# Optimization experiments

Hardware: AMD Instinct MI355X
Metric: run time of the kernel (lower is better)

## Reference

```python
import jax, jax.numpy as jnp
import numpy as np

B, T, E, H, M2 = 8, 2048, 256, 2, 134
HD = E // H


def setup_inputs() -> dict:
    key = jax.random.key(0)
    ks = jax.random.split(key, 10)
    s = 0.02
    return {
        "X": jax.random.normal(ks[0], (B, T, E), dtype=jnp.float32),
        "Y": jax.random.uniform(ks[1], (B, M2), dtype=jnp.float32),
        "wpe": s * jax.random.normal(ks[2], (T, E), dtype=jnp.float32),
        "ln1_g": jnp.ones((E,), jnp.float32), "ln1_b": jnp.zeros((E,), jnp.float32),
        "attn_w": s * jax.random.normal(ks[3], (3 * E, E), dtype=jnp.float32),
        "attn_b": jnp.zeros((3 * E,), jnp.float32),
        "attnproj_w": s * jax.random.normal(ks[4], (E, E), dtype=jnp.float32),
        "attnproj_b": jnp.zeros((E,), jnp.float32),
        "ln2_g": jnp.ones((E,), jnp.float32), "ln2_b": jnp.zeros((E,), jnp.float32),
        "fc_w": s * jax.random.normal(ks[5], (2 * E, E), dtype=jnp.float32),
        "fc_b": jnp.zeros((2 * E,), jnp.float32),
        "mlpproj_w": s * jax.random.normal(ks[6], (E, 2 * E), dtype=jnp.float32),
        "mlpproj_b": jnp.zeros((E,), jnp.float32),
        "lnf_g": jnp.ones((E,), jnp.float32), "lnf_b": jnp.zeros((E,), jnp.float32),
        "head_w": s * jax.random.normal(ks[7], (M2, E), dtype=jnp.float32),
        "head_b": jnp.zeros((M2,), jnp.float32),
    }


def _ln(x, g, b, eps=1e-5):
    mu = x.mean(-1, keepdims=True)
    var = ((x - mu) ** 2).mean(-1, keepdims=True)
    return (x - mu) * jax.lax.rsqrt(var + eps) * g + b


def reference(X, Y, wpe, ln1_g, ln1_b, attn_w, attn_b, attnproj_w, attnproj_b,
              ln2_g, ln2_b, fc_w, fc_b, mlpproj_w, mlpproj_b, lnf_g, lnf_b,
              head_w, head_b):
    # positional ids = arange(T) -> wpe itself; cls ids = [0]*T/2 + [1]*T/2
    cls_ids = np.concatenate([np.zeros(T // 2, np.int32), np.ones(T // 2, np.int32)])
    x = X + wpe + wpe[cls_ids]                      # [B,T,E] (dropout = identity, eval)

    # single Block (n_layer=1), preceded by ReLU as in cross_mod loop
    x = jax.nn.relu(x)
    h = _ln(x, ln1_g, ln1_b)
    qkv = h @ attn_w.T + attn_b                     # [B,T,3E]
    q, k, v = jnp.split(qkv, 3, axis=-1)
    q, k, v = jax.nn.relu(q), jax.nn.relu(k), jax.nn.relu(v)
    split_heads = lambda t: t.reshape(B, T, H, HD).transpose(0, 2, 1, 3)
    q, k, v = split_heads(q), split_heads(k), split_heads(v)
    att = jnp.einsum('bhqd,bhkd->bhqk', q, k) * (1.0 / np.sqrt(HD))
    tril = jnp.tril(jnp.ones((T, T), dtype=bool))
    # masked_fill(-inf) then ReLU  ==  zero outside causal mask, ReLU inside
    att = jnp.where(tril, jax.nn.relu(att), 0.0)    # [B,H,T,T]
    y = jnp.einsum('bhqk,bhkd->bhqd', att, v)
    y = y.transpose(0, 2, 1, 3).reshape(B, T, E)
    x = x + (y @ attnproj_w.T + attnproj_b)

    h = _ln(x, ln2_g, ln2_b)
    x = x + (jax.nn.relu(h @ fc_w.T + fc_b) @ mlpproj_w.T + mlpproj_b)

    x = jax.nn.relu(x)
    x = _ln(x, lnf_g, lnf_b)
    x = jax.nn.relu(x)
    emb = x.mean(axis=1)                            # [B,E]
    logits = jax.nn.relu(emb @ head_w.T + head_b)   # [B,M2]

    loss1 = jnp.sqrt(jnp.mean((logits - Y) ** 2))
    e1, e2 = emb[:, : E // 2], emb[:, E // 2:]
    loss3 = jnp.sqrt(jnp.mean((e1 - e2) ** 2))
    loss = 50.0 * loss1 + loss3
    return (e1, e2, loss, loss1, loss3, logits)
```

## Files before the change

### kernel.cpp

```cpp
#include <hip/hip_runtime.h>
#include <hip/hip_bf16.h>

#define Bc 8
#define Tc 2048
#define Ec 256
#define Hc 2
#define HDc 128
#define Mrows (Bc*Tc)
#define M2c 134

using bfx8  = __attribute__((ext_vector_type(8))) __bf16;
using f32x4 = __attribute__((ext_vector_type(4))) float;

__device__ __forceinline__ void gll16(const __bf16* g, __bf16* lds) {
    __builtin_amdgcn_global_load_lds(
        (const __attribute__((address_space(1))) unsigned int*)g,
        (__attribute__((address_space(3))) unsigned int*)lds, 16, 0, 0);
}

__global__ __launch_bounds__(256) void embed_prep_k(const float* X, const float* wpe,
                                                    const float* g, const float* bb,
                                                    const float* attn_w, const float* apw,
                                                    const float* fcw, const float* mpw,
                                                    __bf16* wb, float* embsum,
                                                    __bf16* xres, __bf16* hb) {
    int m = blockIdx.x;
    int e = threadIdx.x;
    if (m < 2048) {
        int i = m * 256 + e;
        if (i < 196608)       wb[i] = (__bf16)attn_w[i];
        else if (i < 262144)  wb[i] = (__bf16)apw[i - 196608];
        else if (i < 393216)  wb[i] = (__bf16)fcw[i - 262144];
        else                  wb[i] = (__bf16)mpw[i - 393216];
        if (m < 8) embsum[m * 256 + e] = 0.f;
    }
    int t = m & (Tc - 1);
    float v = X[(size_t)m * Ec + e] + wpe[(size_t)t * Ec + e] + wpe[(size_t)(t >= 1024) * Ec + e];
    v = fmaxf(v, 0.f);
    xres[(size_t)m * Ec + e] = (__bf16)v;
    float s1 = v, s2 = v * v;
    #pragma unroll
    for (int o = 32; o; o >>= 1) { s1 += __shfl_xor(s1, o, 64); s2 += __shfl_xor(s2, o, 64); }
    __shared__ float a1[4], a2[4];
    int w = threadIdx.x >> 6;
    if ((threadIdx.x & 63) == 0) { a1[w] = s1; a2[w] = s2; }
    __syncthreads();
    float m1 = (a1[0] + a1[1] + a1[2] + a1[3]) * (1.f / 256.f);
    float m2 = (a2[0] + a2[1] + a2[2] + a2[3]) * (1.f / 256.f);
    float r = rsqrtf(m2 - m1 * m1 + 1e-5f);
    hb[(size_t)m * Ec + e] = (__bf16)((v - m1) * r * g[e] + bb[e]);
}

__global__ __launch_bounds__(256) void gemm_qkv(const __bf16* __restrict__ A,
                                                const __bf16* __restrict__ Bw,
                                                const float* __restrict__ bias,
                                                __bf16* __restrict__ Qb,
                                                __bf16* __restrict__ Kb,
                                                __bf16* __restrict__ Vb) {
    const int K = 256;
    __shared__ __bf16 As[128 * 64];
    __shared__ __bf16 Bs[128 * 64];
    const int tid = threadIdx.x, w = tid >> 6, l = tid & 63;
    const int m0 = blockIdx.y * 128, n0 = blockIdx.x * 128;
    const int wr = w >> 1, wc = w & 1;
    const int quad = l >> 4, col15 = l & 15;

    f32x4 acc[4][4];
    f32x4 zz = {0.f, 0.f, 0.f, 0.f};
    #pragma unroll
    for (int i = 0; i < 4; i++)
        #pragma unroll
        for (int j = 0; j < 4; j++) acc[i][j] = zz;

    const int lrow = l >> 3;
    const int pbs  = l & 7;

    for (int kb = 0; kb < K; kb += 64) {
        #pragma unroll
        for (int it = 0; it < 4; it++) {
            int chunk = w * 4 + it;
            int row = chunk * 8 + lrow;
            int lb = pbs ^ (row & 7);
            gll16(A  + (size_t)(m0 + row) * K + kb + lb * 8, As + chunk * 512);
            gll16(Bw + (size_t)(n0 + row) * K + kb + lb * 8, Bs + chunk * 512);
        }
        __syncthreads();
        #pragma unroll
        for (int ks = 0; ks < 2; ks++) {
            bfx8 af[4], bfr[4];
            #pragma unroll
            for (int rt = 0; rt < 4; rt++) {
                int row = wr * 64 + rt * 16 + col15;
                int pb = (ks * 4 + quad) ^ (row & 7);
                af[rt] = *(const bfx8*)(As + row * 64 + pb * 8);
            }
            #pragma unroll
            for (int ct = 0; ct < 4; ct++) {
                int row = wc * 64 + ct * 16 + col15;
                int pb = (ks * 4 + quad) ^ (row & 7);
                bfr[ct] = *(const bfx8*)(Bs + row * 64 + pb * 8);
            }
            #pragma unroll
            for (int rt = 0; rt < 4; rt++)
                #pragma unroll
                for (int ct = 0; ct < 4; ct++)
                    acc[rt][ct] = __builtin_amdgcn_mfma_f32_16x16x32_bf16(af[rt], bfr[ct], acc[rt][ct], 0, 0, 0);
        }
        __syncthreads();
    }

    #pragma unroll
    for (int rt = 0; rt < 4; rt++)
        #pragma unroll
        for (int ct = 0; ct < 4; ct++) {
            int mgb = m0 + wr * 64 + rt * 16 + quad * 4;
            int ng  = n0 + wc * 64 + ct * 16 + col15;
            float bsv = bias[ng];
            #pragma unroll
            for (int r = 0; r < 4; r++) {
                float val = fmaxf(acc[rt][ct][r] + bsv, 0.f);
                int mg = mgb + r;
                int sel = ng >> 8;
                int hh = (ng >> 7) & 1;
                int d = ng & 127;
                int bb = mg >> 11, tt = mg & (Tc - 1);
                size_t idx = ((size_t)((bb * 2 + hh) * Tc + tt)) * HDc + d;
                __bf16 bv = (__bf16)val;
                if (sel == 0) Qb[idx] = bv;
                else if (sel == 1) Kb[idx] = bv;
                else Vb[idx] = bv;
            }
        }
}

__global__ __launch_bounds__(256) void transpose_v(const unsigned short* Vb, unsigned short* Vt) {
    __shared__ unsigned short tile[64][66];
    int kt = blockIdx.x, dt = blockIdx.y, bh = blockIdx.z;
    int tid = threadIdx.x;
    int k0 = kt * 64, d0 = dt * 64;
    int rr = tid >> 4, cc = (tid & 15) * 4;
    #pragma unroll
    for (int p = 0; p < 4; p++) {
        int k = p * 16 + rr;
        const unsigned short* src = Vb + ((size_t)(bh * Tc + k0 + k)) * HDc + d0 + cc;
        ushort4 vv = *(const ushort4*)src;
        tile[k][cc] = vv.x; tile[k][cc + 1] = vv.y; tile[k][cc + 2] = vv.z; tile[k][cc + 3] = vv.w;
    }
    __syncthreads();
    #pragma unroll
    for (int p = 0; p < 4; p++) {
        int d = p * 16 + rr;
        unsigned short* dst = Vt + ((size_t)(bh * HDc + d0 + d)) * Tc + k0 + cc;
        ushort4 ov;
        ov.x = tile[cc][d]; ov.y = tile[cc + 1][d]; ov.z = tile[cc + 2][d]; ov.w = tile[cc + 3][d];
        *(ushort4*)dst = ov;
    }
}

__global__ __launch_bounds__(256, 4) void attn6_k(const __bf16* __restrict__ Qb,
                                                  const __bf16* __restrict__ Kb,
                                                  const __bf16* __restrict__ Vt,
                                                  __bf16* __restrict__ Y1,
                                                  __bf16* __restrict__ Y2,
                                                  __bf16* __restrict__ Y3,
                                                  __bf16* __restrict__ Y4) {
    __shared__ __bf16 Ks[64 * 128];
    __shared__ __bf16 Vs[128 * 64];
    __shared__ __bf16 Ss[64 * 64];
    int bid = blockIdx.x;
    int lane8 = bid & 7;
    int s = bid >> 3;
    int bh = ((s & 1) << 3) | lane8;
    int f = s >> 1;
    int qt, ch;
    if (f < 8)       { qt = f;                    ch = 0; }
    else if (f < 24) { qt = 8 + ((f - 8) >> 1);   ch = (f - 8) & 1; }
    else if (f < 48) { int r = f - 24; int d3 = r / 3; qt = 16 + d3; ch = r - 3 * d3; }
    else             { int r = f - 48; qt = 24 + (r >> 2); ch = r & 3; }
    int Q0 = qt * 64;
    int kts = ch * 8;
    int kte = min(kts + 8, qt + 1);

    int tid = threadIdx.x, w = tid >> 6, l = tid & 63;
    int quad = l >> 4, col15 = l & 15;
    const int lrowK = l >> 4, pbsK = l & 15;
    const int lrowV = l >> 3, pbsV = l & 7;

    #pragma unroll
    for (int it = 0; it < 4; it++) {
        int chunk = w * 4 + it;
        int row = chunk * 4 + lrowK;
        int lb = pbsK ^ (row & 7);
        gll16(Qb + ((size_t)(bh * Tc + Q0 + row)) * HDc + lb * 8, Ks + chunk * 512);
    }
    __syncthreads();
    bfx8 qf[4];
    #pragma unroll
    for (int ks = 0; ks < 4; ks++) {
        int row = w * 16 + col15;
        int pb = (ks * 4 + quad) ^ (row & 7);
        qf[ks] = *(const bfx8*)(Ks + row * 128 + pb * 8);
    }

    f32x4 zz = {0.f, 0.f, 0.f, 0.f};
    f32x4 yacc[8];
    #pragma unroll
    for (int i = 0; i < 8; i++) yacc[i] = zz;

    for (int kt = kts; kt < kte; kt++) {
        __syncthreads();
        #pragma unroll
        for (int it = 0; it < 4; it++) {
            int chunk = w * 4 + it;
            int rowK = chunk * 4 + lrowK;
            int lbK = pbsK ^ (rowK & 7);
            gll16(Kb + ((size_t)(bh * Tc + kt * 64 + rowK)) * HDc + lbK * 8, Ks + chunk * 512);
            int rowV = chunk * 8 + lrowV;
            int lbV = pbsV ^ (rowV & 7);
            gll16(Vt + ((size_t)(bh * HDc + rowV)) * Tc + kt * 64 + lbV * 8, Vs + chunk * 512);
        }
        __syncthreads();

        f32x4 sacc[4];
        #pragma unroll
        for (int i = 0; i < 4; i++) sacc[i] = zz;
        #pragma unroll
        for (int ks = 0; ks < 4; ks++) {
            #pragma unroll
            for (int ct = 0; ct < 4; ct++) {
                int row = ct * 16 + col15;
                int pb = (ks * 4 + quad) ^ (row & 7);
                bfx8 kf = *(const bfx8*)(Ks + row * 128 + pb * 8);
                sacc[ct] = __builtin_amdgcn_mfma_f32_16x16x32_bf16(qf[ks], kf, sacc[ct], 0, 0, 0);
            }
        }

        #pragma unroll
        for (int ct = 0; ct < 4; ct++) {
            int kl = ct * 16 + col15;
            int kg = kt * 64 + kl;
            int blk = kl >> 3, off = kl & 7;
            #pragma unroll
            for (int r = 0; r < 4; r++) {
                int qlw = w * 16 + quad * 4 + r;
                float val = (kg <= Q0 + qlw) ? fmaxf(sacc[ct][r], 0.f) : 0.f;
                int pb = blk ^ (qlw & 7);
                Ss[qlw * 64 + pb * 8 + off] = (__bf16)val;
            }
        }

        #pragma unroll
        for (int ks = 0; ks < 2; ks++) {
            int rowS = w * 16 + col15;
            int pbS = (ks * 4 + quad) ^ (rowS & 7);
            bfx8 sf = *(const bfx8*)(Ss + rowS * 64 + pbS * 8);
            #pragma unroll
            for (int dt = 0; dt < 8; dt++) {
                int row = dt * 16 + col15;
                int pb = (ks * 4 + quad) ^ (row & 7);
                bfx8 vf = *(const bfx8*)(Vs + row * 64 + pb * 8);
                yacc[dt] = __builtin_amdgcn_mfma_f32_16x16x32_bf16(sf, vf, yacc[dt], 0, 0, 0);
            }
        }
    }

    __bf16* Yp = (ch == 0) ? Y1 : (ch == 1) ? Y2 : (ch == 2) ? Y3 : Y4;
    int b = bh >> 1, h = bh & 1;
    const float sc = 0.08838834764831845f;
    #pragma unroll
    for (int dt = 0; dt < 8; dt++) {
        int d = dt * 16 + col15;
        #pragma unroll
        for (int r = 0; r < 4; r++) {
            int q = Q0 + w * 16 + quad * 4 + r;
            Yp[((size_t)(b * Tc + q)) * Ec + h * HDc + d] = (__bf16)(yacc[dt][r] * sc);
        }
    }
}

__global__ __launch_bounds__(256, 1) void mega_k(const __bf16* __restrict__ Y1,
                                                 const __bf16* __restrict__ Y2,
                                                 const __bf16* __restrict__ Y3,
                                                 const __bf16* __restrict__ Y4,
                                                 const __bf16* __restrict__ wap,
                                                 const float* __restrict__ apb,
                                                 const __bf16* __restrict__ xres,
                                                 const float* __restrict__ ln2_g,
                                                 const float* __restrict__ ln2_b,
                                                 const __bf16* __restrict__ wfc,
                                                 const float* __restrict__ fcb,
                                                 const __bf16* __restrict__ wmp,
                                                 const float* __restrict__ mpb,
                                                 const float* __restrict__ lnf_g,
                                                 const float* __restrict__ lnf_b,
                                                 float* __restrict__ embsum) {
    __shared__ __bf16 h2s[4 * 4096];
    __shared__ __bf16 fc64[8 * 4096];
    __shared__ __bf16 Bs[256 * 64];
    __shared__ float cs[256];
    const int tid = threadIdx.x, w = tid >> 6, l = tid & 63;
    const int m0 = blockIdx.x * 64;
    const int quad = l >> 4, col15 = l & 15;
    const int lrow = l >> 3, pbs = l & 7;
    f32x4 zz = {0.f, 0.f, 0.f, 0.f};
    cs[tid] = 0.f;

    int nsum = (((m0 & (Tc - 1)) >> 6) + 8) >> 3;
    const __bf16* Ys[4] = {Y1, Y2, Y3, Y4};
    __bf16* As = fc64;

    f32x4 acc[16];
    #pragma unroll
    for (int i = 0; i < 16; i++) acc[i] = zz;

    for (int kb = 0; kb < 256; kb += 64) {
        bfx8 av[2]; int rows[2], blks[2];
        #pragma unroll
        for (int it = 0; it < 2; it++) {
            int idx = it * 256 + tid;
            int row = idx >> 3, blk = idx & 7;
            rows[it] = row; blks[it] = blk;
            size_t off = (size_t)(m0 + row) * 256 + kb + blk * 8;
            bfx8 a1 = *(const bfx8*)(Y1 + off);
            float tmp[8];
            #pragma unroll
            for (int jj = 0; jj < 8; jj++) tmp[jj] = (float)a1[jj];
            for (int j = 1; j < nsum; j++) {
                bfx8 aj = *(const bfx8*)(Ys[j] + off);
                #pragma unroll
                for (int jj = 0; jj < 8; jj++) tmp[jj] += (float)aj[jj];
            }
            #pragma unroll
            for (int jj = 0; jj < 8; jj++) a1[jj] = (__bf16)tmp[jj];
            av[it] = a1;
        }
        __syncthreads();
        #pragma unroll
        for (int it = 0; it < 2; it++) {
            int row = rows[it];
            int pb = blks[it] ^ (row & 7);
            *(bfx8*)(As + row * 64 + pb * 8) = av[it];
        }
        #pragma unroll
        for (int it = 0; it < 8; it++) {
            int chunk = w * 8 + it;
            int row = chunk * 8 + lrow;
            int lb = pbs ^ (row & 7);
            gll16(wap + (size_t)row * 256 + kb + lb * 8, Bs + chunk * 512);
        }
        __syncthreads();
        #pragma unroll
        for (int ks = 0; ks < 2; ks++) {
            int arow = w * 16 + col15;
            int apbk = (ks * 4 + quad) ^ (arow & 7);
            bfx8 af = *(const bfx8*)(As + arow * 64 + apbk * 8);
            #pragma unroll
            for (int ct = 0; ct < 16; ct++) {
                int brow = ct * 16 + col15;
                int bpb = (ks * 4 + quad) ^ (brow & 7);
                bfx8 bf = *(const bfx8*)(Bs + brow * 64 + bpb * 8);
                acc[ct] = __builtin_amdgcn_mfma_f32_16x16x32_bf16(af, bf, acc[ct], 0, 0, 0);
            }
        }
    }

    float xv[16][4];
    #pragma unroll
    for (int ct = 0; ct < 16; ct++) {
        int ng = ct * 16 + col15;
        float bsv = apb[ng];
        #pragma unroll
        for (int r = 0; r < 4; r++) {
            int mg = m0 + w * 16 + quad * 4 + r;
            xv[ct][r] = acc[ct][r] + bsv + (float)xres[(size_t)mg * 256 + ng];
        }
    }
    {
        float s1[4], s2[4];
        #pragma unroll
        for (int r = 0; r < 4; r++) {
            float a = 0.f, b2 = 0.f;
            #pragma unroll
            for (int ct = 0; ct < 16; ct++) { a += xv[ct][r]; b2 += xv[ct][r] * xv[ct][r]; }
            #pragma unroll
            for (int o = 1; o < 16; o <<= 1) { a += __shfl_xor(a, o, 64); b2 += __shfl_xor(b2, o, 64); }
            s1[r] = a; s2[r] = b2;
        }
        #pragma unroll
        for (int r = 0; r < 4; r++) {
            float mu = s1[r] * (1.f / 256.f);
            float var = s2[r] * (1.f / 256.f) - mu * mu;
            float rs = rsqrtf(var + 1e-5f);
            int row = w * 16 + quad * 4 + r;
            #pragma unroll
            for (int ct = 0; ct < 16; ct++) {
                int ng = ct * 16 + col15;
                float h = (xv[ct][r] - mu) * rs * ln2_g[ng] + ln2_b[ng];
                int panel = ng >> 6, c = ng & 63;
                h2s[panel * 4096 + row * 64 + ((c >> 3) ^ (row & 7)) * 8 + (c & 7)] = (__bf16)h;
            }
        }
    }

    for (int half = 0; half < 2; half++) {
        f32x4 acc2[16];
        #pragma unroll
        for (int i = 0; i < 16; i++) acc2[i] = zz;
        for (int kb = 0; kb < 256; kb += 64) {
            __syncthreads();
            #pragma unroll
            for (int it = 0; it < 8; it++) {
                int chunk = w * 8 + it;
                int row = chunk * 8 + lrow;
                int lb = pbs ^ (row & 7);
                gll16(wfc + (size_t)(half * 256 + row) * 256 + kb + lb * 8, Bs + chunk * 512);
            }
            __syncthreads();
            int panel = kb >> 6;
            #pragma unroll
            for (int ks = 0; ks < 2; ks++) {
                int arow = w * 16 + col15;
                int apbk = (ks * 4 + quad) ^ (arow & 7);
                bfx8 af = *(const bfx8*)(h2s + panel * 4096 + arow * 64 + apbk * 8);
                #pragma unroll
                for (int ct = 0; ct < 16; ct++) {
                    int brow = ct * 16 + col15;
                    int bpb = (ks * 4 + quad) ^ (brow & 7);
                    bfx8 bf = *(const bfx8*)(Bs + brow * 64 + bpb * 8);
                    acc2[ct] = __builtin_amdgcn_mfma_f32_16x16x32_bf16(af, bf, acc2[ct], 0, 0, 0);
                }
            }
        }
        #pragma unroll
        for (int ct = 0; ct < 16; ct++) {
            int col = half * 256 + ct * 16 + col15;
            float bsv = fcb[col];
            int panel = col >> 6, c = col & 63;
            #pragma unroll
            for (int r = 0; r < 4; r++) {
                int row = w * 16 + quad * 4 + r;
                float val = fmaxf(acc2[ct][r] + bsv, 0.f);
                fc64[panel * 4096 + row * 64 + ((c >> 3) ^ (row & 7)) * 8 + (c & 7)] = (__bf16)val;
            }
        }
    }

    #pragma unroll
    for (int i = 0; i < 16; i++) acc[i] = zz;
    for (int kb = 0; kb < 512; kb += 64) {
        __syncthreads();
        #pragma unroll
        for (int it = 0; it < 8; it++) {
            int chunk = w * 8 + it;
            int row = chunk * 8 + lrow;
            int lb = pbs ^ (row & 7);
            gll16(wmp + (size_t)row * 512 + kb + lb * 8, Bs + chunk * 512);
        }
        __syncthreads();
        int panel = kb >> 6;
        #pragma unroll
        for (int ks = 0; ks < 2; ks++) {
            int arow = w * 16 + col15;
            int apbk = (ks * 4 + quad) ^ (arow & 7);
            bfx8 af = *(const bfx8*)(fc64 + panel * 4096 + arow * 64 + apbk * 8);
            #pragma unroll
            for (int ct = 0; ct < 16; ct++) {
                int brow = ct * 16 + col15;
                int bpb = (ks * 4 + quad) ^ (brow & 7);
                bfx8 bf = *(const bfx8*)(Bs + brow * 64 + bpb * 8);
                acc[ct] = __builtin_amdgcn_mfma_f32_16x16x32_bf16(af, bf, acc[ct], 0, 0, 0);
            }
        }
    }

    #pragma unroll
    for (int ct = 0; ct < 16; ct++) {
        int ng = ct * 16 + col15;
        float bsv = mpb[ng];
        #pragma unroll
        for (int r = 0; r < 4; r++)
            xv[ct][r] = fmaxf(acc[ct][r] + bsv + xv[ct][r], 0.f);
    }
    float s1[4], s2[4];
    #pragma unroll
    for (int r = 0; r < 4; r++) {
        float a = 0.f, b2 = 0.f;
        #pragma unroll
        for (int ct = 0; ct < 16; ct++) { a += xv[ct][r]; b2 += xv[ct][r] * xv[ct][r]; }
        #pragma unroll
        for (int o = 1; o < 16; o <<= 1) { a += __shfl_xor(a, o, 64); b2 += __shfl_xor(b2, o, 64); }
        s1[r] = a; s2[r] = b2;
    }
    float colsum[16];
    #pragma unroll
    for (int ct = 0; ct < 16; ct++) colsum[ct] = 0.f;
    #pragma unroll
    for (int r = 0; r < 4; r++) {
        float mu = s1[r] * (1.f / 256.f);
        float var = s2[r] * (1.f / 256.f) - mu * mu;
        float rs = rsqrtf(var + 1e-5f);
        #pragma unroll
        for (int ct = 0; ct < 16; ct++) {
            int ng = ct * 16 + col15;
            float h = (xv[ct][r] - mu) * rs * lnf_g[ng] + lnf_b[ng];
            colsum[ct] += fmaxf(h, 0.f);
        }
    }
    #pragma unroll
    for (int ct = 0; ct < 16; ct++) {
        colsum[ct] += __shfl_xor(colsum[ct], 16, 64);
        colsum[ct] += __shfl_xor(colsum[ct], 32, 64);
    }
    if (quad == 0) {
        #pragma unroll
        for (int ct = 0; ct < 16; ct++)
            atomicAdd(&cs[ct * 16 + col15], colsum[ct]);
    }
    __syncthreads();
    atomicAdd(&embsum[(m0 >> 11) * 256 + tid], cs[tid]);
}

__global__ __launch_bounds__(256) void final_k(const float* embsum, const float* Yt,
                                               const float* head_w, const float* head_b,
                                               float* out) {
    __shared__ float semb[2048];
    __shared__ float slog[1072];
    int tid = threadIdx.x;
    for (int i = tid; i < 2048; i += 256) semb[i] = embsum[i] * (1.f / 2048.f);
    __syncthreads();
    float part1 = 0.f;
    for (int idx = tid; idx < 1072; idx += 256) {
        int b = idx / M2c, n = idx - b * M2c;
        float acc = head_b[n];
        const float* wn = head_w + (size_t)n * Ec;
        const float* e = semb + b * Ec;
        #pragma unroll 8
        for (int k = 0; k < Ec; k++) acc += e[k] * wn[k];
        acc = fmaxf(acc, 0.f);
        slog[idx] = acc;
        float d = acc - Yt[idx];
        part1 += d * d;
    }
    float part3 = 0.f;
    for (int idx = tid; idx < 1024; idx += 256) {
        int b = idx >> 7, i = idx & 127;
        float d = semb[b * Ec + i] - semb[b * Ec + 128 + i];
        part3 += d * d;
    }
    #pragma unroll
    for (int o = 32; o; o >>= 1) { part1 += __shfl_xor(part1, o, 64); part3 += __shfl_xor(part3, o, 64); }
    __shared__ float r1[4], r3[4];
    int w = tid >> 6;
    if ((tid & 63) == 0) { r1[w] = part1; r3[w] = part3; }
    __syncthreads();
    float l1 = sqrtf((r1[0] + r1[1] + r1[2] + r1[3]) / 1072.f);
    float l3 = sqrtf((r3[0] + r3[1] + r3[2] + r3[3]) / 1024.f);
    for (int idx = tid; idx < 1024; idx += 256) {
        int b = idx >> 7, i = idx & 127;
        out[idx]        = semb[b * Ec + i];
        out[1024 + idx] = semb[b * Ec + 128 + i];
    }
    if (tid == 0) {
        out[2048] = 50.f * l1 + l3;
        out[2049] = l1;
        out[2050] = l3;
    }
    for (int idx = tid; idx < 1072; idx += 256) out[2051 + idx] = slog[idx];
}

extern "C" void kernel_launch(void* const* d_in, const int* in_sizes, int n_in,
                              void* d_out, int out_size, void* d_ws, size_t ws_size,
                              hipStream_t stream) {
    const float* X        = (const float*)d_in[0];
    const float* Yt       = (const float*)d_in[1];
    const float* wpe      = (const float*)d_in[2];
    const float* ln1_g    = (const float*)d_in[3];
    const float* ln1_b    = (const float*)d_in[4];
    const float* attn_w   = (const float*)d_in[5];
    const float* attn_b   = (const float*)d_in[6];
    const float* apw      = (const float*)d_in[7];
    const float* apb      = (const float*)d_in[8];
    const float* ln2_g    = (const float*)d_in[9];
    const float* ln2_b    = (const float*)d_in[10];
    const float* fcw      = (const float*)d_in[11];
    const float* fcb      = (const float*)d_in[12];
    const float* mpw      = (const float*)d_in[13];
    const float* mpb      = (const float*)d_in[14];
    const float* lnf_g    = (const float*)d_in[15];
    const float* lnf_b    = (const float*)d_in[16];
    const float* head_w   = (const float*)d_in[17];
    const float* head_b   = (const float*)d_in[18];

    char* ws = (char*)d_ws;
    const size_t MB = 1048576;
    __bf16* xres   = (__bf16*)(ws + 0 * MB);
    __bf16* hb     = (__bf16*)(ws + 8 * MB);
    __bf16* Qb     = (__bf16*)(ws + 16 * MB);
    __bf16* Kb     = (__bf16*)(ws + 24 * MB);
    __bf16* Vb     = (__bf16*)(ws + 32 * MB);
    __bf16* Vt     = (__bf16*)(ws + 40 * MB);
    __bf16* Y1     = (__bf16*)(ws + 48 * MB);
    __bf16* Y2     = (__bf16*)(ws + 56 * MB);
    __bf16* wb     = (__bf16*)(ws + 64 * MB);
    float*  embsum = (float*)(ws + 65 * MB);

    __bf16* Y3 = hb;
    __bf16* Y4 = Vb;

    __bf16* wqkv = wb;
    __bf16* wap  = wb + 196608;
    __bf16* wfc  = wb + 262144;
    __bf16* wmp  = wb + 393216;

    embed_prep_k<<<Mrows, 256, 0, stream>>>(X, wpe, ln1_g, ln1_b,
                                            attn_w, apw, fcw, mpw, wb, embsum, xres, hb);
    gemm_qkv<<<dim3(6, 128), 256, 0, stream>>>(hb, wqkv, attn_b, Qb, Kb, Vb);
    transpose_v<<<dim3(32, 2, 16), 256, 0, stream>>>((const unsigned short*)Vb, (unsigned short*)Vt);
    attn6_k<<<1280, 256, 0, stream>>>(Qb, Kb, Vt, Y1, Y2, Y3, Y4);
    mega_k<<<256, 256, 0, stream>>>(Y1, Y2, Y3, Y4, wap, apb, xres, ln2_g, ln2_b,
                                    wfc, fcb, wmp, mpb, lnf_g, lnf_b, embsum);
    final_k<<<1, 256, 0, stream>>>(embsum, Yt, head_w, head_b, (float*)d_out);
}
```

Baseline: 249.3 us.

## Split mega_k column work across 8 waves and prefetch summed Y tiles

The fused post-attention kernel now runs 512 threads per block. Each of the 8 waves owns a 32-column slice across all 64 rows, where before each of 4 waves owned 16 rows across all 256 columns. LayerNorm statistics are now reduced across waves through shared memory, and the summed Y partials for the next k-block are loaded while the current block computes. This raises the number of waves available to hide MFMA and memory latency, at the cost of extra barriers, shared-memory reductions, and more A-fragment loads per wave.

```diff
diff --git a/kernel.cpp b/kernel.cpp
--- a/kernel.cpp
+++ b/kernel.cpp
@@ -278,7 +278,7 @@
     }
 }
 
-__global__ __launch_bounds__(256, 1) void mega_k(const __bf16* __restrict__ Y1,
+__global__ __launch_bounds__(512, 1) void mega_k(const __bf16* __restrict__ Y1,
                                                  const __bf16* __restrict__ Y2,
                                                  const __bf16* __restrict__ Y3,
                                                  const __bf16* __restrict__ Y4,
@@ -297,120 +297,147 @@
     __shared__ __bf16 h2s[4 * 4096];
     __shared__ __bf16 fc64[8 * 4096];
     __shared__ __bf16 Bs[256 * 64];
-    __shared__ float cs[256];
+    __shared__ float ps1[64][8], ps2[64][8];
+    __shared__ float mus[64], rss[64];
     const int tid = threadIdx.x, w = tid >> 6, l = tid & 63;
     const int m0 = blockIdx.x * 64;
     const int quad = l >> 4, col15 = l & 15;
     const int lrow = l >> 3, pbs = l & 7;
+    const int n0 = w * 32;
     f32x4 zz = {0.f, 0.f, 0.f, 0.f};
-    cs[tid] = 0.f;
-
-    int nsum = (((m0 & (Tc - 1)) >> 6) + 8) >> 3;
-    const __bf16* Ys[4] = {Y1, Y2, Y3, Y4};
+
+    const int nsum = (((m0 & (Tc - 1)) >> 6) + 8) >> 3;
     __bf16* As = fc64;
 
-    f32x4 acc[16];
-    #pragma unroll
-    for (int i = 0; i < 16; i++) acc[i] = zz;
+    const int arow_s = tid >> 3;
+    const int ablk   = tid & 7;
+
+    auto loadY = [&](int kb) -> bfx8 {
+        size_t off = (size_t)(m0 + arow_s) * 256 + kb + ablk * 8;
+        bfx8 a1 = *(const bfx8*)(Y1 + off);
+        float tmp[8];
+        #pragma unroll
+        for (int jj = 0; jj < 8; jj++) tmp[jj] = (float)a1[jj];
+        if (nsum > 1) { bfx8 aj = *(const bfx8*)(Y2 + off);
+            #pragma unroll
+            for (int jj = 0; jj < 8; jj++) tmp[jj] += (float)aj[jj]; }
+        if (nsum > 2) { bfx8 aj = *(const bfx8*)(Y3 + off);
+            #pragma unroll
+            for (int jj = 0; jj < 8; jj++) tmp[jj] += (float)aj[jj]; }
+        if (nsum > 3) { bfx8 aj = *(const bfx8*)(Y4 + off);
+            #pragma unroll
+            for (int jj = 0; jj < 8; jj++) tmp[jj] += (float)aj[jj]; }
+        #pragma unroll
+        for (int jj = 0; jj < 8; jj++) a1[jj] = (__bf16)tmp[jj];
+        return a1;
+    };
+
+    f32x4 acc[4][2];
+    #pragma unroll
+    for (int rt = 0; rt < 4; rt++)
+        #pragma unroll
+        for (int ct = 0; ct < 2; ct++) acc[rt][ct] = zz;
+
+    bfx8 av = loadY(0);
 
     for (int kb = 0; kb < 256; kb += 64) {
-        bfx8 av[2]; int rows[2], blks[2];
-        #pragma unroll
-        for (int it = 0; it < 2; it++) {
-            int idx = it * 256 + tid;
-            int row = idx >> 3, blk = idx & 7;
-            rows[it] = row; blks[it] = blk;
-            size_t off = (size_t)(m0 + row) * 256 + kb + blk * 8;
-            bfx8 a1 = *(const bfx8*)(Y1 + off);
-            float tmp[8];
-            #pragma unroll
-            for (int jj = 0; jj < 8; jj++) tmp[jj] = (float)a1[jj];
-            for (int j = 1; j < nsum; j++) {
-                bfx8 aj = *(const bfx8*)(Ys[j] + off);
-                #pragma unroll
-                for (int jj = 0; jj < 8; jj++) tmp[jj] += (float)aj[jj];
-            }
-            #pragma unroll
-            for (int jj = 0; jj < 8; jj++) a1[jj] = (__bf16)tmp[jj];
-            av[it] = a1;
-        }
-        __syncthreads();
-        #pragma unroll
-        for (int it = 0; it < 2; it++) {
-            int row = rows[it];
-            int pb = blks[it] ^ (row & 7);
-            *(bfx8*)(As + row * 64 + pb * 8) = av[it];
-        }
-        #pragma unroll
-        for (int it = 0; it < 8; it++) {
-            int chunk = w * 8 + it;
+        __syncthreads();
+        { int pb = ablk ^ (arow_s & 7);
+          *(bfx8*)(As + arow_s * 64 + pb * 8) = av; }
+        #pragma unroll
+        for (int it = 0; it < 4; it++) {
+            int chunk = w * 4 + it;
             int row = chunk * 8 + lrow;
             int lb = pbs ^ (row & 7);
             gll16(wap + (size_t)row * 256 + kb + lb * 8, Bs + chunk * 512);
         }
+        bfx8 avn;
+        if (kb < 192) avn = loadY(kb + 64);
         __syncthreads();
         #pragma unroll
         for (int ks = 0; ks < 2; ks++) {
-            int arow = w * 16 + col15;
-            int apbk = (ks * 4 + quad) ^ (arow & 7);
-            bfx8 af = *(const bfx8*)(As + arow * 64 + apbk * 8);
-            #pragma unroll
-            for (int ct = 0; ct < 16; ct++) {
-                int brow = ct * 16 + col15;
-                int bpb = (ks * 4 + quad) ^ (brow & 7);
-                bfx8 bf = *(const bfx8*)(Bs + brow * 64 + bpb * 8);
-                acc[ct] = __builtin_amdgcn_mfma_f32_16x16x32_bf16(af, bf, acc[ct], 0, 0, 0);
-            }
-        }
-    }
-
-    float xv[16][4];
-    #pragma unroll
-    for (int ct = 0; ct < 16; ct++) {
-        int ng = ct * 16 + col15;
+            bfx8 af[4];
+            #pragma unroll
+            for (int rt = 0; rt < 4; rt++) {
+                int ar = rt * 16 + col15;
+                int apbk = (ks * 4 + quad) ^ (ar & 7);
+                af[rt] = *(const bfx8*)(As + ar * 64 + apbk * 8);
+            }
+            #pragma unroll
+            for (int ct = 0; ct < 2; ct++) {
+                int br = n0 + ct * 16 + col15;
+                int bpb = (ks * 4 + quad) ^ (br & 7);
+                bfx8 bf = *(const bfx8*)(Bs + br * 64 + bpb * 8);
+                #pragma unroll
+                for (int rt = 0; rt < 4; rt++)
+                    acc[rt][ct] = __builtin_amdgcn_mfma_f32_16x16x32_bf16(af[rt], bf, acc[rt][ct], 0, 0, 0);
+            }
+        }
+        if (kb < 192) av = avn;
+    }
+
+    float xv[4][2][4];
+    #pragma unroll
+    for (int ct = 0; ct < 2; ct++) {
+        int ng = n0 + ct * 16 + col15;
         float bsv = apb[ng];
         #pragma unroll
+        for (int rt = 0; rt < 4; rt++)
+            #pragma unroll
+            for (int r = 0; r < 4; r++) {
+                int mg = m0 + rt * 16 + quad * 4 + r;
+                xv[rt][ct][r] = acc[rt][ct][r] + bsv + (float)xres[(size_t)mg * 256 + ng];
+            }
+    }
+    #pragma unroll
+    for (int rt = 0; rt < 4; rt++)
+        #pragma unroll
         for (int r = 0; r < 4; r++) {
-            int mg = m0 + w * 16 + quad * 4 + r;
-            xv[ct][r] = acc[ct][r] + bsv + (float)xres[(size_t)mg * 256 + ng];
-        }
-    }
+            float a  = xv[rt][0][r] + xv[rt][1][r];
+            float b2 = xv[rt][0][r] * xv[rt][0][r] + xv[rt][1][r] * xv[rt][1][r];
+            #pragma unroll
+            for (int o = 1; o < 16; o <<= 1) { a += __shfl_xor(a, o, 64); b2 += __shfl_xor(b2, o, 64); }
+            if (col15 == 0) { int row = rt * 16 + quad * 4 + r; ps1[row][w] = a; ps2[row][w] = b2; }
+        }
+    __syncthreads();
     {
-        float s1[4], s2[4];
-        #pragma unroll
-        for (int r = 0; r < 4; r++) {
-            float a = 0.f, b2 = 0.f;
-            #pragma unroll
-            for (int ct = 0; ct < 16; ct++) { a += xv[ct][r]; b2 += xv[ct][r] * xv[ct][r]; }
-            #pragma unroll
-            for (int o = 1; o < 16; o <<= 1) { a += __shfl_xor(a, o, 64); b2 += __shfl_xor(b2, o, 64); }
-            s1[r] = a; s2[r] = b2;
-        }
-        #pragma unroll
-        for (int r = 0; r < 4; r++) {
-            float mu = s1[r] * (1.f / 256.f);
-            float var = s2[r] * (1.f / 256.f) - mu * mu;
-            float rs = rsqrtf(var + 1e-5f);
-            int row = w * 16 + quad * 4 + r;
-            #pragma unroll
-            for (int ct = 0; ct < 16; ct++) {
-                int ng = ct * 16 + col15;
-                float h = (xv[ct][r] - mu) * rs * ln2_g[ng] + ln2_b[ng];
-                int panel = ng >> 6, c = ng & 63;
+        int row = tid >> 3, widx = tid & 7;
+        float a = ps1[row][widx], b2 = ps2[row][widx];
+        #pragma unroll
+        for (int o = 1; o < 8; o <<= 1) { a += __shfl_xor(a, o, 64); b2 += __shfl_xor(b2, o, 64); }
+        if ((l & 7) == 0) {
+            float mu = a * (1.f / 256.f);
+            float var = b2 * (1.f / 256.f) - mu * mu;
+            mus[row] = mu; rss[row] = rsqrtf(var + 1e-5f);
+        }
+    }
+    __syncthreads();
+    #pragma unroll
+    for (int ct = 0; ct < 2; ct++) {
+        int ng = n0 + ct * 16 + col15;
+        float gv = ln2_g[ng], bv = ln2_b[ng];
+        int panel = ng >> 6, c = ng & 63;
+        #pragma unroll
+        for (int rt = 0; rt < 4; rt++)
+            #pragma unroll
+            for (int r = 0; r < 4; r++) {
+                int row = rt * 16 + quad * 4 + r;
+                float h = (xv[rt][ct][r] - mus[row]) * rss[row] * gv + bv;
                 h2s[panel * 4096 + row * 64 + ((c >> 3) ^ (row & 7)) * 8 + (c & 7)] = (__bf16)h;
             }
-        }
     }
 
     for (int half = 0; half < 2; half++) {
-        f32x4 acc2[16];
-        #pragma unroll
-        for (int i = 0; i < 16; i++) acc2[i] = zz;
+        f32x4 acc2[4][2];
+        #pragma unroll
+        for (int rt = 0; rt < 4; rt++)
+            #pragma unroll
+            for (int ct = 0; ct < 2; ct++) acc2[rt][ct] = zz;
         for (int kb = 0; kb < 256; kb += 64) {
             __syncthreads();
             #pragma unroll
-            for (int it = 0; it < 8; it++) {
-                int chunk = w * 8 + it;
+            for (int it = 0; it < 4; it++) {
+                int chunk = w * 4 + it;
                 int row = chunk * 8 + lrow;
                 int lb = pbs ^ (row & 7);
                 gll16(wfc + (size_t)(half * 256 + row) * 256 + kb + lb * 8, Bs + chunk * 512);
@@ -419,39 +446,49 @@
             int panel = kb >> 6;
             #pragma unroll
             for (int ks = 0; ks < 2; ks++) {
-                int arow = w * 16 + col15;
-                int apbk = (ks * 4 + quad) ^ (arow & 7);
-                bfx8 af = *(const bfx8*)(h2s + panel * 4096 + arow * 64 + apbk * 8);
+                bfx8 af[4];
                 #pragma unroll
-                for (int ct = 0; ct < 16; ct++) {
-                    int brow = ct * 16 + col15;
-                    int bpb = (ks * 4 + quad) ^ (brow & 7);
-                    bfx8 bf = *(const bfx8*)(Bs + brow * 64 + bpb * 8);
-                    acc2[ct] = __builtin_amdgcn_mfma_f32_16x16x32_bf16(af, bf, acc2[ct], 0, 0, 0);
+                for (int rt = 0; rt < 4; rt++) {
+                    int ar = rt * 16 + col15;
+                    int apbk = (ks * 4 + quad) ^ (ar & 7);
+                    af[rt] = *(const bfx8*)(h2s + panel * 4096 + ar * 64 + apbk * 8);
                 }
-            }
-        }
-        #pragma unroll
-        for (int ct = 0; ct < 16; ct++) {
-            int col = half * 256 + ct * 16 + col15;
+                #pragma unroll
+                for (int ct = 0; ct < 2; ct++) {
+                    int br = n0 + ct * 16 + col15;
+                    int bpb = (ks * 4 + quad) ^ (br & 7);
+                    bfx8 bf = *(const bfx8*)(Bs + br * 64 + bpb * 8);
+                    #pragma unroll
+                    for (int rt = 0; rt < 4; rt++)
+                        acc2[rt][ct] = __builtin_amdgcn_mfma_f32_16x16x32_bf16(af[rt], bf, acc2[rt][ct], 0, 0, 0);
+                }
+            }
+        }
+        #pragma unroll
+        for (int ct = 0; ct < 2; ct++) {
+            int col = half * 256 + n0 + ct * 16 + col15;
             float bsv = fcb[col];
             int panel = col >> 6, c = col & 63;
             #pragma unroll
-            for (int r = 0; r < 4; r++) {
-                int row = w * 16 + quad * 4 + r;
-                float val = fmaxf(acc2[ct][r] + bsv, 0.f);
-                fc64[panel * 4096 + row * 64 + ((c >> 3) ^ (row & 7)) * 8 + (c & 7)] = (__bf16)val;
-            }
-        }
-    }
-
-    #pragma unroll
-    for (int i = 0; i < 16; i++) acc[i] = zz;
+            for (int rt = 0; rt < 4; rt++)
+                #pragma unroll
+                for (int r = 0; r < 4; r++) {
+                    int row = rt * 16 + quad * 4 + r;
+                    float val = fmaxf(acc2[rt][ct][r] + bsv, 0.f);
+                    fc64[panel * 4096 + row * 64 + ((c >> 3) ^ (row & 7)) * 8 + (c & 7)] = (__bf16)val;
+                }
+        }
+    }
+
+    #pragma unroll
+    for (int rt = 0; rt < 4; rt++)
+        #pragma unroll
+        for (int ct = 0; ct < 2; ct++) acc[rt][ct] = zz;
     for (int kb = 0; kb < 512; kb += 64) {
         __syncthreads();
         #pragma unroll
-        for (int it = 0; it < 8; it++) {
-            int chunk = w * 8 + it;
+        for (int it = 0; it < 4; it++) {
+            int chunk = w * 4 + it;
             int row = chunk * 8 + lrow;
             int lb = pbs ^ (row & 7);
             gll16(wmp + (size_t)row * 512 + kb + lb * 8, Bs + chunk * 512);
@@ -460,64 +497,75 @@
         int panel = kb >> 6;
         #pragma unroll
         for (int ks = 0; ks < 2; ks++) {
-            int arow = w * 16 + col15;
-            int apbk = (ks * 4 + quad) ^ (arow & 7);
-            bfx8 af = *(const bfx8*)(fc64 + panel * 4096 + arow * 64 + apbk * 8);
-            #pragma unroll
-            for (int ct = 0; ct < 16; ct++) {
-                int brow = ct * 16 + col15;
-                int bpb = (ks * 4 + quad) ^ (brow & 7);
-                bfx8 bf = *(const bfx8*)(Bs + brow * 64 + bpb * 8);
-                acc[ct] = __builtin_amdgcn_mfma_f32_16x16x32_bf16(af, bf, acc[ct], 0, 0, 0);
-            }
-        }
-    }
-
-    #pragma unroll
-    for (int ct = 0; ct < 16; ct++) {
-        int ng = ct * 16 + col15;
+            bfx8 af[4];
+            #pragma unroll
+            for (int rt = 0; rt < 4; rt++) {
+                int ar = rt * 16 + col15;
+                int apbk = (ks * 4 + quad) ^ (ar & 7);
+                af[rt] = *(const bfx8*)(fc64 + panel * 4096 + ar * 64 + apbk * 8);
+            }
+            #pragma unroll
+            for (int ct = 0; ct < 2; ct++) {
+                int br = n0 + ct * 16 + col15;
+                int bpb = (ks * 4 + quad) ^ (br & 7);
+                bfx8 bf = *(const bfx8*)(Bs + br * 64 + bpb * 8);
+                #pragma unroll
+                for (int rt = 0; rt < 4; rt++)
+                    acc[rt][ct] = __builtin_amdgcn_mfma_f32_16x16x32_bf16(af[rt], bf, acc[rt][ct], 0, 0, 0);
+            }
+        }
+    }
+
+    #pragma unroll
+    for (int ct = 0; ct < 2; ct++) {
+        int ng = n0 + ct * 16 + col15;
         float bsv = mpb[ng];
         #pragma unroll
-        for (int r = 0; r < 4; r++)
-            xv[ct][r] = fmaxf(acc[ct][r] + bsv + xv[ct][r], 0.f);
-    }
-    float s1[4], s2[4];
-    #pragma unroll
-    for (int r = 0; r < 4; r++) {
-        float a = 0.f, b2 = 0.f;
-        #pragma unroll
-        for (int ct = 0; ct < 16; ct++) { a += xv[ct][r]; b2 += xv[ct][r] * xv[ct][r]; }
-        #pragma unroll
-        for (int o = 1; o < 16; o <<= 1) { a += __shfl_xor(a, o, 64); b2 += __shfl_xor(b2, o, 64); }
-        s1[r] = a; s2[r] = b2;
-    }
-    float colsum[16];
-    #pragma unroll
-    for (int ct = 0; ct < 16; ct++) colsum[ct] = 0.f;
-    #pragma unroll
-    for (int r = 0; r < 4; r++) {
-        float mu = s1[r] * (1.f / 256.f);
-        float var = s2[r] * (1.f / 256.f) - mu * mu;
-        float rs = rsqrtf(var + 1e-5f);
-        #pragma unroll
-        for (int ct = 0; ct < 16; ct++) {
-            int ng = ct * 16 + col15;
-            float h = (xv[ct][r] - mu) * rs * lnf_g[ng] + lnf_b[ng];
-            colsum[ct] += fmaxf(h, 0.f);
-        }
-    }
-    #pragma unroll
-    for (int ct = 0; ct < 16; ct++) {
-        colsum[ct] += __shfl_xor(colsum[ct], 16, 64);
-        colsum[ct] += __shfl_xor(colsum[ct], 32, 64);
-    }
-    if (quad == 0) {
-        #pragma unroll
-        for (int ct = 0; ct < 16; ct++)
-            atomicAdd(&cs[ct * 16 + col15], colsum[ct]);
-    }
-    __syncthreads();
-    atomicAdd(&embsum[(m0 >> 11) * 256 + tid], cs[tid]);
+        for (int rt = 0; rt < 4; rt++)
+            #pragma unroll
+            for (int r = 0; r < 4; r++)
+                xv[rt][ct][r] = fmaxf(acc[rt][ct][r] + bsv + xv[rt][ct][r], 0.f);
+    }
+    #pragma unroll
+    for (int rt = 0; rt < 4; rt++)
+        #pragma unroll
+        for (int r = 0; r < 4; r++) {
+            float a  = xv[rt][0][r] + xv[rt][1][r];
+            float b2 = xv[rt][0][r] * xv[rt][0][r] + xv[rt][1][r] * xv[rt][1][r];
+            #pragma unroll
+            for (int o = 1; o < 16; o <<= 1) { a += __shfl_xor(a, o, 64); b2 += __shfl_xor(b2, o, 64); }
+            if (col15 == 0) { int row = rt * 16 + quad * 4 + r; ps1[row][w] = a; ps2[row][w] = b2; }
+        }
+    __syncthreads();
+    {
+        int row = tid >> 3, widx = tid & 7;
+        float a = ps1[row][widx], b2 = ps2[row][widx];
+        #pragma unroll
+        for (int o = 1; o < 8; o <<= 1) { a += __shfl_xor(a, o, 64); b2 += __shfl_xor(b2, o, 64); }
+        if ((l & 7) == 0) {
+            float mu = a * (1.f / 256.f);
+            float var = b2 * (1.f / 256.f) - mu * mu;
+            mus[row] = mu; rss[row] = rsqrtf(var + 1e-5f);
+        }
+    }
+    __syncthreads();
+    #pragma unroll
+    for (int ct = 0; ct < 2; ct++) {
+        int ng = n0 + ct * 16 + col15;
+        float gv = lnf_g[ng], bv = lnf_b[ng];
+        float csum = 0.f;
+        #pragma unroll
+        for (int rt = 0; rt < 4; rt++)
+            #pragma unroll
+            for (int r = 0; r < 4; r++) {
+                int row = rt * 16 + quad * 4 + r;
+                float h = (xv[rt][ct][r] - mus[row]) * rss[row] * gv + bv;
+                csum += fmaxf(h, 0.f);
+            }
+        csum += __shfl_xor(csum, 16, 64);
+        csum += __shfl_xor(csum, 32, 64);
+        if (quad == 0) atomicAdd(&embsum[(m0 >> 11) * 256 + ng], csum);
+    }
 }
 
 __global__ __launch_bounds__(256) void final_k(const float* embsum, const float* Yt,
@@ -617,7 +665,7 @@
     gemm_qkv<<<dim3(6, 128), 256, 0, stream>>>(hb, wqkv, attn_b, Qb, Kb, Vb);
     transpose_v<<<dim3(32, 2, 16), 256, 0, stream>>>((const unsigned short*)Vb, (unsigned short*)Vt);
     attn6_k<<<1280, 256, 0, stream>>>(Qb, Kb, Vt, Y1, Y2, Y3, Y4);
-    mega_k<<<256, 256, 0, stream>>>(Y1, Y2, Y3, Y4, wap, apb, xres, ln2_g, ln2_b,
+    mega_k<<<256, 512, 0, stream>>>(Y1, Y2, Y3, Y4, wap, apb, xres, ln2_g, ln2_b,
                                     wfc, fcb, wmp, mpb, lnf_g, lnf_b, embsum);
     final_k<<<1, 256, 0, stream>>>(embsum, Yt, head_w, head_b, (float*)d_out);
 }
```

New measurement: 232.7 us. 1.07x faster.
